# Optimization experiments

Measured on AMD Instinct MI355X. Metric: run time of the kernel, lower is better.

Reference implementation:

```python
import jax, jax.numpy as jnp
import numpy as np

MASK_GROUP = 8
RATIO = 0.125
K = max(1, min(MASK_GROUP, round(RATIO * MASK_GROUP)))  # = 1


def sparify_mask(outM):
    # top-k over the mask_group axis, scatter 1.0 at top-k positions
    _, idx = jax.lax.top_k(outM, K)              # [..., K]
    oh = jax.nn.one_hot(idx, outM.shape[-1], dtype=outM.dtype)  # [..., K, G]
    return jnp.sum(oh, axis=-2)                   # [..., G] 0/1 mask


def setup_inputs() -> dict:
    key = jax.random.key(0)
    ks = jax.random.split(key, 7)
    B, S, D, F = 4, 2048, 2048, 8192
    stdv = 1.0 / np.sqrt(F)
    u = lambda k, shape: jax.random.uniform(k, shape, jnp.float32, -stdv, stdv)
    return {
        "x": jax.random.normal(ks[0], (B, S, D), jnp.float32),
        "W1": u(ks[1], (F, D)),
        "b1": u(ks[2], (F,)),
        "Wm": u(ks[3], (MASK_GROUP, D)),
        "bm": u(ks[4], (MASK_GROUP,)),
        "W2": u(ks[5], (D, F)),
        "b2": u(ks[6], (D,)),
    }


def reference(x, W1, b1, Wm, bm, W2, b2):
    F_out = W1.shape[0]
    repeat_num = F_out // MASK_GROUP
    outL = jnp.einsum('bsd,fd->bsf', x, W1) + b1          # [B,S,F]
    outM = jax.nn.softmax(jnp.einsum('bsd,gd->bsg', x, Wm) + bm, axis=-1)  # [B,S,G]
    mask = sparify_mask(outM)                              # [B,S,G]
    gate = jnp.repeat(mask, repeat_num, axis=-1)           # [B,S,F]
    out2 = jax.nn.relu(outL * gate)
    out = jnp.einsum('bsf,df->bsd', out2, W2) + b2         # [B,S,D]
    return out
```

## Files before the change

### kernel.cpp

```cpp
#include <hip/hip_runtime.h>
#include <hip/hip_bf16.h>

#define T_TOK 8192
#define D_DIM 2048
#define F_DIM 8192
#define G_NUM 8
#define GF    1024

typedef __attribute__((ext_vector_type(8))) short bf16x8;
typedef __attribute__((ext_vector_type(4))) float f32x4;

__device__ __forceinline__ void async_load16(const void* g, void* l) {
    __builtin_amdgcn_global_load_lds(
        (const __attribute__((address_space(1))) unsigned int*)g,
        (__attribute__((address_space(3))) unsigned int*)l, 16, 0, 0);
}

__device__ __forceinline__ unsigned short f2bf(float f) {
    unsigned int u = __float_as_uint(f);
    unsigned int r = (u + 0x7fffu + ((u >> 16) & 1u)) >> 16;
    return (unsigned short)r;
}

__device__ __forceinline__ uint2 pack4(float4 v) {
    union { __hip_bfloat162 b; unsigned u; } c0, c1;
    c0.b = __float22bfloat162_rn({v.x, v.y});
    c1.b = __float22bfloat162_rn({v.z, v.w});
    uint2 r; r.x = c0.u; r.y = c1.u; return r;
}


__global__ void zero_cnt_kernel(int* __restrict__ cnt) {
    if (threadIdx.x < G_NUM) cnt[threadIdx.x] = 0;
}

__global__ __launch_bounds__(256)
void convert_kernel(const float* __restrict__ src, unsigned short* __restrict__ dst, int n) {
    int i = (blockIdx.x * 256 + threadIdx.x) * 8;
    if (i >= n) return;
    float4 a = *(const float4*)(src + i);
    float4 b = *(const float4*)(src + i + 4);
    uint2 p0 = pack4(a), p1 = pack4(b);
    uint4 o; o.x = p0.x; o.y = p0.y; o.z = p1.x; o.w = p1.y;
    *(uint4*)(dst + i) = o;
}

template <bool WRITE_XB>
__global__ __launch_bounds__(64)
void gate_partial_kernel(const float* __restrict__ x, const float* __restrict__ Wm,
                         unsigned short* __restrict__ xb, double* __restrict__ part) {
    const int q     = blockIdx.x;
    const int t     = blockIdx.y;
    const int lane  = threadIdx.x;
    const int tok0  = t * 64;
    const int kbase = q * 512;

    __shared__ float wmS[8][512];
    __shared__ float xs[64][68];

    for (int i = lane * 4; i < 8 * 512; i += 64 * 4) {
        int g = i >> 9, d = i & 511;
        *(float4*)&wmS[g][d] = *(const float4*)(Wm + (size_t)g * D_DIM + kbase + d);
    }

    double acc[8] = {0, 0, 0, 0, 0, 0, 0, 0};

    const int srow = lane >> 2;
    const int scol = (lane & 3) * 4;

    float4 v[16];
#define LOAD_CHUNK(dbase_)                                                        \
    _Pragma("unroll") for (int it = 0; it < 4; ++it)                              \
    _Pragma("unroll") for (int ci = 0; ci < 4; ++ci) {                            \
        int row = it * 16 + srow;                                                 \
        int col = ci * 16 + scol;                                                 \
        v[it * 4 + ci] = *(const float4*)(x + (size_t)(tok0 + row) * D_DIM +      \
                                          kbase + (dbase_) + col);                \
    }

    LOAD_CHUNK(0)
    __syncthreads();

    for (int s = 0; s < 8; ++s) {
        const int dbase = s * 64;
#pragma unroll
        for (int it = 0; it < 4; ++it)
#pragma unroll
            for (int ci = 0; ci < 4; ++ci) {
                int row = it * 16 + srow;
                int col = ci * 16 + scol;
                *(float4*)&xs[row][col] = v[it * 4 + ci];
                if (WRITE_XB) {
                    uint2 p = pack4(v[it * 4 + ci]);
                    *(uint2*)(xb + (size_t)(tok0 + row) * D_DIM + kbase + dbase + col) = p;
                }
            }
        __syncthreads();
        if (s < 7) { LOAD_CHUNK(dbase + 64) }
#pragma unroll
        for (int j4 = 0; j4 < 16; ++j4) {
            float4 xv = *(const float4*)&xs[lane][j4 * 4];
#pragma unroll
            for (int g = 0; g < 8; ++g) {
                float4 wv = *(const float4*)&wmS[g][dbase + j4 * 4];
                acc[g] += (double)xv.x * (double)wv.x;
                acc[g] += (double)xv.y * (double)wv.y;
                acc[g] += (double)xv.z * (double)wv.z;
                acc[g] += (double)xv.w * (double)wv.w;
            }
        }
        __syncthreads();
    }
#undef LOAD_CHUNK

    double* dst = part + (((size_t)t * 4 + q) * 64 + lane) * 8;
#pragma unroll
    for (int g = 0; g < 8; ++g) dst[g] = acc[g];
}

__global__ __launch_bounds__(256)
void gate_combine_kernel(const double* __restrict__ part, const float* __restrict__ bm,
                         int* __restrict__ cnt, int* __restrict__ bucket) {
    int tok = blockIdx.x * 256 + threadIdx.x;
    int t = tok >> 6, L = tok & 63;
    double s[8];
#pragma unroll
    for (int g = 0; g < 8; ++g) s[g] = (double)bm[g];
#pragma unroll
    for (int q = 0; q < 4; ++q) {
        const double* p = part + (((size_t)t * 4 + q) * 64 + L) * 8;
#pragma unroll
        for (int g = 0; g < 8; ++g) s[g] += p[g];
    }
    double best = s[0]; int bg = 0;
#pragma unroll
    for (int g = 1; g < 8; ++g)
        if (s[g] > best) { best = s[g]; bg = g; }
    int pos = atomicAdd(&cnt[bg], 1);
    bucket[bg * T_TOK + pos] = tok;
}

template <int KDIM, bool IS_G1, bool A_BF16, bool B_BF16>
__global__ __launch_bounds__(256)
void mfma_gemm(const void* __restrict__ Aop, const void* __restrict__ Bop,
               const float* __restrict__ bias,
               const int* __restrict__ cnt, const int* __restrict__ bucket,
               unsigned short* __restrict__ outH, float* __restrict__ outF) {
    const int g  = blockIdx.z;
    const int n  = cnt[g];
    const int t0 = blockIdx.y * 128;
    if (t0 >= n) return;
    const int nx0 = blockIdx.x * 128;
    const int tid  = threadIdx.x;
    const int lane = tid & 63;
    const int wv   = tid >> 6;

    __shared__ int toks[128];
    __shared__ __align__(16) unsigned short As[128 * 32];
    __shared__ __align__(16) unsigned short Bs[128 * 32];

    if (tid < 128) {
        int r = t0 + tid;
        if (r >= n) r = n - 1;
        toks[tid] = bucket[g * T_TOK + r];
    }
    __syncthreads();

    const size_t bstride = IS_G1 ? (size_t)KDIM : (size_t)F_DIM;
    const size_t brow0   = IS_G1 ? (size_t)(g * GF + nx0) : (size_t)nx0;
    const size_t bcol    = IS_G1 ? 0 : (size_t)(g * GF);

    const int lrow = tid >> 2;
    const int lseg = tid & 3;
    const unsigned short* aP0 = nullptr; const unsigned short* aP1 = nullptr;
    const unsigned short* bP0 = nullptr; const unsigned short* bP1 = nullptr;
    char *ldsA0 = nullptr, *ldsA1 = nullptr, *ldsB0 = nullptr, *ldsB1 = nullptr;
    if (A_BF16) {
        const unsigned short* Ab = (const unsigned short*)Aop;
        aP0 = Ab + (size_t)toks[lrow] * KDIM + lseg * 8;
        aP1 = Ab + (size_t)toks[64 + lrow] * KDIM + lseg * 8;
        ldsA0 = (char*)As + tid * 16;
        ldsA1 = (char*)As + 4096 + tid * 16;
    }
    if (B_BF16) {
        const unsigned short* Bb = (const unsigned short*)Bop;
        bP0 = Bb + (brow0 + lrow) * bstride + bcol + lseg * 8;
        bP1 = Bb + (brow0 + 64 + lrow) * bstride + bcol + lseg * 8;
        ldsB0 = (char*)Bs + tid * 16;
        ldsB1 = (char*)Bs + 4096 + tid * 16;
    }

    const int frw = tid >> 1;
    const int fsg = (tid & 1) * 16;
    const float* aF = nullptr; const float* bF = nullptr;
    char *ldsAf = nullptr, *ldsBf = nullptr;
    if (!A_BF16) {
        aF = (const float*)Aop + (size_t)toks[frw] * KDIM + fsg;
        ldsAf = (char*)As + frw * 64 + (tid & 1) * 32;
    }
    if (!B_BF16) {
        bF = (const float*)Bop + (brow0 + frw) * bstride + bcol + fsg;
        ldsBf = (char*)Bs + frw * 64 + (tid & 1) * 32;
    }

    f32x4 acc[4][4];
#pragma unroll
    for (int mi = 0; mi < 4; ++mi)
#pragma unroll
        for (int ni = 0; ni < 4; ++ni)
            acc[mi][ni] = (f32x4){0.f, 0.f, 0.f, 0.f};

    const int wr   = (wv >> 1) * 64;
    const int wc   = (wv & 1) * 64;
    const int frow = lane & 15;
    const int kh   = lane >> 4;

    for (int k0 = 0; k0 < KDIM; k0 += 32) {
        __syncthreads();
        if (A_BF16) { async_load16(aP0 + k0, ldsA0); async_load16(aP1 + k0, ldsA1); }
        if (B_BF16) { async_load16(bP0 + k0, ldsB0); async_load16(bP1 + k0, ldsB1); }
        if (!A_BF16) {
            float4 v0 = *(const float4*)(aF + k0);
            float4 v1 = *(const float4*)(aF + k0 + 4);
            float4 v2 = *(const float4*)(aF + k0 + 8);
            float4 v3 = *(const float4*)(aF + k0 + 12);
            uint2 p0 = pack4(v0), p1 = pack4(v1), p2 = pack4(v2), p3 = pack4(v3);
            uint4 w0; w0.x = p0.x; w0.y = p0.y; w0.z = p1.x; w0.w = p1.y;
            uint4 w1; w1.x = p2.x; w1.y = p2.y; w1.z = p3.x; w1.w = p3.y;
            *(uint4*)ldsAf = w0; *(uint4*)(ldsAf + 16) = w1;
        }
        if (!B_BF16) {
            float4 v0 = *(const float4*)(bF + k0);
            float4 v1 = *(const float4*)(bF + k0 + 4);
            float4 v2 = *(const float4*)(bF + k0 + 8);
            float4 v3 = *(const float4*)(bF + k0 + 12);
            uint2 p0 = pack4(v0), p1 = pack4(v1), p2 = pack4(v2), p3 = pack4(v3);
            uint4 w0; w0.x = p0.x; w0.y = p0.y; w0.z = p1.x; w0.w = p1.y;
            uint4 w1; w1.x = p2.x; w1.y = p2.y; w1.z = p3.x; w1.w = p3.y;
            *(uint4*)ldsBf = w0; *(uint4*)(ldsBf + 16) = w1;
        }
        __syncthreads();
        bf16x8 af[4], bfr[4];
#pragma unroll
        for (int mi = 0; mi < 4; ++mi)
            af[mi] = *(const bf16x8*)((const char*)As + (size_t)(wr + mi * 16 + frow) * 64 + kh * 16);
#pragma unroll
        for (int ni = 0; ni < 4; ++ni)
            bfr[ni] = *(const bf16x8*)((const char*)Bs + (size_t)(wc + ni * 16 + frow) * 64 + kh * 16);
#pragma unroll
        for (int mi = 0; mi < 4; ++mi)
#pragma unroll
            for (int ni = 0; ni < 4; ++ni)
                acc[mi][ni] = __builtin_amdgcn_mfma_f32_16x16x32_bf16(
                    af[mi], bfr[ni], acc[mi][ni], 0, 0, 0);
    }

    const float* bptr = bias + (IS_G1 ? (g * GF + nx0) : nx0);
    float bv[4];
#pragma unroll
    for (int ni = 0; ni < 4; ++ni) bv[ni] = bptr[wc + ni * 16 + frow];

#pragma unroll
    for (int mi = 0; mi < 4; ++mi) {
#pragma unroll
        for (int v = 0; v < 4; ++v) {
            int r = wr + mi * 16 + kh * 4 + v;
            if (t0 + r < n) {
                int tok = toks[r];
                if (IS_G1) {
                    unsigned short* dst = outH + (size_t)tok * GF + nx0 + wc + frow;
#pragma unroll
                    for (int ni = 0; ni < 4; ++ni) {
                        float o = fmaxf(acc[mi][ni][v] + bv[ni], 0.f);
                        dst[ni * 16] = f2bf(o);
                    }
                } else {
                    float* dst = outF + (size_t)tok * D_DIM + nx0 + wc + frow;
#pragma unroll
                    for (int ni = 0; ni < 4; ++ni)
                        dst[ni * 16] = acc[mi][ni][v] + bv[ni];
                }
            }
        }
    }
}

extern "C" void kernel_launch(void* const* d_in, const int* in_sizes, int n_in,
                              void* d_out, int out_size, void* d_ws, size_t ws_size,
                              hipStream_t stream) {
    const float* x  = (const float*)d_in[0];
    const float* W1 = (const float*)d_in[1];
    const float* b1 = (const float*)d_in[2];
    const float* Wm = (const float*)d_in[3];
    const float* bm = (const float*)d_in[4];
    const float* W2 = (const float*)d_in[5];
    const float* b2 = (const float*)d_in[6];
    float* out = (float*)d_out;

    int* cnt    = (int*)d_ws;
    int* bucket = (int*)((char*)d_ws + 1024);
    double* part = (double*)((char*)d_ws + (1 << 19));
    unsigned short* Hb  = (unsigned short*)((char*)d_ws + (1 << 19));
    unsigned short* xb  = Hb  + (size_t)T_TOK * GF;
    unsigned short* W1b = xb  + (size_t)T_TOK * D_DIM;
    unsigned short* W2b = W1b + (size_t)F_DIM * D_DIM;

    const bool fast = ws_size >= 117964800ull;
    const bool mid  = ws_size >= 50855936ull;
    const int NCVT = T_TOK * D_DIM;

    zero_cnt_kernel<<<1, 64, 0, stream>>>(cnt);
    if (fast || mid)
        gate_partial_kernel<true><<<dim3(4, 128), 64, 0, stream>>>(x, Wm, xb, part);
    else
        gate_partial_kernel<false><<<dim3(4, 128), 64, 0, stream>>>(x, Wm, nullptr, part);
    gate_combine_kernel<<<T_TOK / 256, 256, 0, stream>>>(part, bm, cnt, bucket);

    if (fast) {
        convert_kernel<<<NCVT / (256 * 8), 256, 0, stream>>>(W1, W1b, NCVT);
        convert_kernel<<<NCVT / (256 * 8), 256, 0, stream>>>(W2, W2b, NCVT);
        mfma_gemm<D_DIM, true, true, true><<<dim3(GF / 128, T_TOK / 128, G_NUM), 256, 0, stream>>>(
            xb, W1b, b1, cnt, bucket, Hb, nullptr);
        mfma_gemm<GF, false, true, true><<<dim3(D_DIM / 128, T_TOK / 128, G_NUM), 256, 0, stream>>>(
            Hb, W2b, b2, cnt, bucket, nullptr, out);
    } else if (mid) {
        mfma_gemm<D_DIM, true, true, false><<<dim3(GF / 128, T_TOK / 128, G_NUM), 256, 0, stream>>>(
            xb, W1, b1, cnt, bucket, Hb, nullptr);
        mfma_gemm<GF, false, true, false><<<dim3(D_DIM / 128, T_TOK / 128, G_NUM), 256, 0, stream>>>(
            Hb, W2, b2, cnt, bucket, nullptr, out);
    } else {
        mfma_gemm<D_DIM, true, false, false><<<dim3(GF / 128, T_TOK / 128, G_NUM), 256, 0, stream>>>(
            x, W1, b1, cnt, bucket, Hb, nullptr);
        mfma_gemm<GF, false, true, false><<<dim3(D_DIM / 128, T_TOK / 128, G_NUM), 256, 0, stream>>>(
            Hb, W2, b2, cnt, bucket, nullptr, out);
    }
}
```

Before: 405.0 us.

## Widen GEMM K-tile to 64 with XOR-swizzled LDS, remap tiles, split gate wider

The grouped MFMA GEMM now stages a 64-wide K slice per iteration, which halves the barrier count. LDS rows are XOR-swizzled to avoid bank conflicts on the fragment reads. Block indices are remapped so neighbouring blocks share token tiles for better L2 reuse. The gate partial kernel splits D into 16 chunks instead of 4 for more parallelism, and the combine kernel now sums 16 partials. In exchange, LDS use doubles per block, which may lower occupancy.

```diff
diff --git a/kernel.cpp b/kernel.cpp
--- a/kernel.cpp
+++ b/kernel.cpp
@@ -6,6 +6,8 @@
 #define F_DIM 8192
 #define G_NUM 8
 #define GF    1024
+#define GATE_Q 16
+#define GATE_D 128
 
 typedef __attribute__((ext_vector_type(8))) short bf16x8;
 typedef __attribute__((ext_vector_type(4))) float f32x4;
@@ -27,6 +29,18 @@
     c0.b = __float22bfloat162_rn({v.x, v.y});
     c1.b = __float22bfloat162_rn({v.z, v.w});
     uint2 r; r.x = c0.u; r.y = c1.u; return r;
+}
+
+__device__ __forceinline__ void stage_f32_64(const float* src, char* rowBase,
+                                             int sbase, int rmask) {
+#pragma unroll
+    for (int i = 0; i < 4; ++i) {
+        float4 v0 = *(const float4*)(src + i * 8);
+        float4 v1 = *(const float4*)(src + i * 8 + 4);
+        uint2 p0 = pack4(v0), p1 = pack4(v1);
+        uint4 w; w.x = p0.x; w.y = p0.y; w.z = p1.x; w.w = p1.y;
+        *(uint4*)(rowBase + ((sbase + i) ^ rmask) * 16) = w;
+    }
 }
 
 
@@ -53,13 +67,13 @@
     const int t     = blockIdx.y;
     const int lane  = threadIdx.x;
     const int tok0  = t * 64;
-    const int kbase = q * 512;
-
-    __shared__ float wmS[8][512];
+    const int kbase = q * GATE_D;
+
+    __shared__ float wmS[8][GATE_D];
     __shared__ float xs[64][68];
 
-    for (int i = lane * 4; i < 8 * 512; i += 64 * 4) {
-        int g = i >> 9, d = i & 511;
+    for (int i = lane * 4; i < 8 * GATE_D; i += 64 * 4) {
+        int g = i >> 7, d = i & (GATE_D - 1);
         *(float4*)&wmS[g][d] = *(const float4*)(Wm + (size_t)g * D_DIM + kbase + d);
     }
 
@@ -81,7 +95,7 @@
     LOAD_CHUNK(0)
     __syncthreads();
 
-    for (int s = 0; s < 8; ++s) {
+    for (int s = 0; s < 2; ++s) {
         const int dbase = s * 64;
 #pragma unroll
         for (int it = 0; it < 4; ++it)
@@ -96,7 +110,7 @@
                 }
             }
         __syncthreads();
-        if (s < 7) { LOAD_CHUNK(dbase + 64) }
+        if (s < 1) { LOAD_CHUNK(dbase + 64) }
 #pragma unroll
         for (int j4 = 0; j4 < 16; ++j4) {
             float4 xv = *(const float4*)&xs[lane][j4 * 4];
@@ -113,22 +127,22 @@
     }
 #undef LOAD_CHUNK
 
-    double* dst = part + (((size_t)t * 4 + q) * 64 + lane) * 8;
+    double* dst = part + (((size_t)t * GATE_Q + q) * 64 + lane) * 8;
 #pragma unroll
     for (int g = 0; g < 8; ++g) dst[g] = acc[g];
 }
 
-__global__ __launch_bounds__(256)
+__global__ __launch_bounds__(64)
 void gate_combine_kernel(const double* __restrict__ part, const float* __restrict__ bm,
                          int* __restrict__ cnt, int* __restrict__ bucket) {
-    int tok = blockIdx.x * 256 + threadIdx.x;
+    int tok = blockIdx.x * 64 + threadIdx.x;
     int t = tok >> 6, L = tok & 63;
     double s[8];
 #pragma unroll
     for (int g = 0; g < 8; ++g) s[g] = (double)bm[g];
 #pragma unroll
-    for (int q = 0; q < 4; ++q) {
-        const double* p = part + (((size_t)t * 4 + q) * 64 + L) * 8;
+    for (int q = 0; q < GATE_Q; ++q) {
+        const double* p = part + (((size_t)t * GATE_Q + q) * 64 + L) * 8;
 #pragma unroll
         for (int g = 0; g < 8; ++g) s[g] += p[g];
     }
@@ -148,16 +162,18 @@
                unsigned short* __restrict__ outH, float* __restrict__ outF) {
     const int g  = blockIdx.z;
     const int n  = cnt[g];
-    const int t0 = blockIdx.y * 128;
+    constexpr int NX = IS_G1 ? (GF / 128) : (D_DIM / 128);
+    const int l = blockIdx.y * NX + blockIdx.x;
+    const int t0  = ((l & 7) + 8 * (l / (8 * NX))) * 128;
+    const int nx0 = ((l >> 3) % NX) * 128;
     if (t0 >= n) return;
-    const int nx0 = blockIdx.x * 128;
     const int tid  = threadIdx.x;
     const int lane = tid & 63;
     const int wv   = tid >> 6;
 
     __shared__ int toks[128];
-    __shared__ __align__(16) unsigned short As[128 * 32];
-    __shared__ __align__(16) unsigned short Bs[128 * 32];
+    __shared__ __align__(16) unsigned short As[128 * 64];
+    __shared__ __align__(16) unsigned short Bs[128 * 64];
 
     if (tid < 128) {
         int r = t0 + tid;
@@ -170,38 +186,31 @@
     const size_t brow0   = IS_G1 ? (size_t)(g * GF + nx0) : (size_t)nx0;
     const size_t bcol    = IS_G1 ? 0 : (size_t)(g * GF);
 
-    const int lrow = tid >> 2;
-    const int lseg = tid & 3;
-    const unsigned short* aP0 = nullptr; const unsigned short* aP1 = nullptr;
-    const unsigned short* bP0 = nullptr; const unsigned short* bP1 = nullptr;
-    char *ldsA0 = nullptr, *ldsA1 = nullptr, *ldsB0 = nullptr, *ldsB1 = nullptr;
+    const int arow = tid >> 3;
+    const int segg = (tid & 7) ^ (arow & 7);
+    const unsigned short* aP[4]; const unsigned short* bP[4];
+    char* ldsA = (char*)As + tid * 16;
+    char* ldsB = (char*)Bs + tid * 16;
     if (A_BF16) {
         const unsigned short* Ab = (const unsigned short*)Aop;
-        aP0 = Ab + (size_t)toks[lrow] * KDIM + lseg * 8;
-        aP1 = Ab + (size_t)toks[64 + lrow] * KDIM + lseg * 8;
-        ldsA0 = (char*)As + tid * 16;
-        ldsA1 = (char*)As + 4096 + tid * 16;
+#pragma unroll
+        for (int j = 0; j < 4; ++j)
+            aP[j] = Ab + (size_t)toks[arow + 32 * j] * KDIM + segg * 8;
     }
     if (B_BF16) {
         const unsigned short* Bb = (const unsigned short*)Bop;
-        bP0 = Bb + (brow0 + lrow) * bstride + bcol + lseg * 8;
-        bP1 = Bb + (brow0 + 64 + lrow) * bstride + bcol + lseg * 8;
-        ldsB0 = (char*)Bs + tid * 16;
-        ldsB1 = (char*)Bs + 4096 + tid * 16;
+#pragma unroll
+        for (int j = 0; j < 4; ++j)
+            bP[j] = Bb + (brow0 + arow + 32 * j) * bstride + bcol + segg * 8;
     }
 
     const int frw = tid >> 1;
-    const int fsg = (tid & 1) * 16;
+    const int fs  = tid & 1;
     const float* aF = nullptr; const float* bF = nullptr;
-    char *ldsAf = nullptr, *ldsBf = nullptr;
-    if (!A_BF16) {
-        aF = (const float*)Aop + (size_t)toks[frw] * KDIM + fsg;
-        ldsAf = (char*)As + frw * 64 + (tid & 1) * 32;
-    }
-    if (!B_BF16) {
-        bF = (const float*)Bop + (brow0 + frw) * bstride + bcol + fsg;
-        ldsBf = (char*)Bs + frw * 64 + (tid & 1) * 32;
-    }
+    char* ldsAf = (char*)As + frw * 128;
+    char* ldsBf = (char*)Bs + frw * 128;
+    if (!A_BF16) aF = (const float*)Aop + (size_t)toks[frw] * KDIM + fs * 32;
+    if (!B_BF16) bF = (const float*)Bop + (brow0 + frw) * bstride + bcol + fs * 32;
 
     f32x4 acc[4][4];
 #pragma unroll
@@ -214,45 +223,40 @@
     const int wc   = (wv & 1) * 64;
     const int frow = lane & 15;
     const int kh   = lane >> 4;
-
-    for (int k0 = 0; k0 < KDIM; k0 += 32) {
+    const int xm   = frow & 7;
+    const char* aBase = (const char*)As + (size_t)(wr + frow) * 128;
+    const char* bBase = (const char*)Bs + (size_t)(wc + frow) * 128;
+
+    for (int k0 = 0; k0 < KDIM; k0 += 64) {
         __syncthreads();
-        if (A_BF16) { async_load16(aP0 + k0, ldsA0); async_load16(aP1 + k0, ldsA1); }
-        if (B_BF16) { async_load16(bP0 + k0, ldsB0); async_load16(bP1 + k0, ldsB1); }
-        if (!A_BF16) {
-            float4 v0 = *(const float4*)(aF + k0);
-            float4 v1 = *(const float4*)(aF + k0 + 4);
-            float4 v2 = *(const float4*)(aF + k0 + 8);
-            float4 v3 = *(const float4*)(aF + k0 + 12);
-            uint2 p0 = pack4(v0), p1 = pack4(v1), p2 = pack4(v2), p3 = pack4(v3);
-            uint4 w0; w0.x = p0.x; w0.y = p0.y; w0.z = p1.x; w0.w = p1.y;
-            uint4 w1; w1.x = p2.x; w1.y = p2.y; w1.z = p3.x; w1.w = p3.y;
-            *(uint4*)ldsAf = w0; *(uint4*)(ldsAf + 16) = w1;
-        }
-        if (!B_BF16) {
-            float4 v0 = *(const float4*)(bF + k0);
-            float4 v1 = *(const float4*)(bF + k0 + 4);
-            float4 v2 = *(const float4*)(bF + k0 + 8);
-            float4 v3 = *(const float4*)(bF + k0 + 12);
-            uint2 p0 = pack4(v0), p1 = pack4(v1), p2 = pack4(v2), p3 = pack4(v3);
-            uint4 w0; w0.x = p0.x; w0.y = p0.y; w0.z = p1.x; w0.w = p1.y;
-            uint4 w1; w1.x = p2.x; w1.y = p2.y; w1.z = p3.x; w1.w = p3.y;
-            *(uint4*)ldsBf = w0; *(uint4*)(ldsBf + 16) = w1;
-        }
+        if (A_BF16) {
+#pragma unroll
+            for (int j = 0; j < 4; ++j) async_load16(aP[j] + k0, ldsA + j * 4096);
+        }
+        if (B_BF16) {
+#pragma unroll
+            for (int j = 0; j < 4; ++j) async_load16(bP[j] + k0, ldsB + j * 4096);
+        }
+        if (!A_BF16) stage_f32_64(aF + k0, ldsAf, fs * 4, frw & 7);
+        if (!B_BF16) stage_f32_64(bF + k0, ldsBf, fs * 4, frw & 7);
         __syncthreads();
-        bf16x8 af[4], bfr[4];
-#pragma unroll
-        for (int mi = 0; mi < 4; ++mi)
-            af[mi] = *(const bf16x8*)((const char*)As + (size_t)(wr + mi * 16 + frow) * 64 + kh * 16);
-#pragma unroll
-        for (int ni = 0; ni < 4; ++ni)
-            bfr[ni] = *(const bf16x8*)((const char*)Bs + (size_t)(wc + ni * 16 + frow) * 64 + kh * 16);
-#pragma unroll
-        for (int mi = 0; mi < 4; ++mi)
+#pragma unroll
+        for (int kk = 0; kk < 2; ++kk) {
+            const int so = ((kk * 4 + kh) ^ xm) * 16;
+            bf16x8 af[4], bfr[4];
+#pragma unroll
+            for (int mi = 0; mi < 4; ++mi)
+                af[mi] = *(const bf16x8*)(aBase + mi * 2048 + so);
 #pragma unroll
             for (int ni = 0; ni < 4; ++ni)
-                acc[mi][ni] = __builtin_amdgcn_mfma_f32_16x16x32_bf16(
-                    af[mi], bfr[ni], acc[mi][ni], 0, 0, 0);
+                bfr[ni] = *(const bf16x8*)(bBase + ni * 2048 + so);
+#pragma unroll
+            for (int mi = 0; mi < 4; ++mi)
+#pragma unroll
+                for (int ni = 0; ni < 4; ++ni)
+                    acc[mi][ni] = __builtin_amdgcn_mfma_f32_16x16x32_bf16(
+                        af[mi], bfr[ni], acc[mi][ni], 0, 0, 0);
+        }
     }
 
     const float* bptr = bias + (IS_G1 ? (g * GF + nx0) : nx0);
@@ -311,10 +315,10 @@
 
     zero_cnt_kernel<<<1, 64, 0, stream>>>(cnt);
     if (fast || mid)
-        gate_partial_kernel<true><<<dim3(4, 128), 64, 0, stream>>>(x, Wm, xb, part);
+        gate_partial_kernel<true><<<dim3(GATE_Q, 128), 64, 0, stream>>>(x, Wm, xb, part);
     else
-        gate_partial_kernel<false><<<dim3(4, 128), 64, 0, stream>>>(x, Wm, nullptr, part);
-    gate_combine_kernel<<<T_TOK / 256, 256, 0, stream>>>(part, bm, cnt, bucket);
+        gate_partial_kernel<false><<<dim3(GATE_Q, 128), 64, 0, stream>>>(x, Wm, nullptr, part);
+    gate_combine_kernel<<<T_TOK / 64, 64, 0, stream>>>(part, bm, cnt, bucket);
 
     if (fast) {
         convert_kernel<<<NCVT / (256 * 8), 256, 0, stream>>>(W1, W1b, NCVT);
```

Result: slower. 420.1 us (+3.7%).

## Split gate reduction finer and launch grouped GEMMs from a compact tile list

Applied to the files above, without the earlier changes.

The gate partial kernel now splits the D reduction into 16 slices of 128 instead of 4 slices of 512, so it launches four times as many blocks, and the combine kernel sums the extra partials. A new single-thread kernel builds a compact list of (group, token-tile) entries from the per-group counts. Both grouped GEMMs launch only MAX_TILES rows of blocks indexed through that list, instead of a full 3D grid where most blocks exit early. The changes aim to fill the GPU during the fp64 gating pass and to cut idle block scheduling in the GEMMs. The cost is a larger partials buffer, an extra serial planning launch and more combine work.

```diff
diff --git a/kernel.cpp b/kernel.cpp
--- a/kernel.cpp
+++ b/kernel.cpp
@@ -6,6 +6,9 @@
 #define F_DIM 8192
 #define G_NUM 8
 #define GF    1024
+#define GATE_Q 16
+#define GATE_D 128
+#define MAX_TILES 72
 
 typedef __attribute__((ext_vector_type(8))) short bf16x8;
 typedef __attribute__((ext_vector_type(4))) float f32x4;
@@ -32,6 +35,17 @@
 
 __global__ void zero_cnt_kernel(int* __restrict__ cnt) {
     if (threadIdx.x < G_NUM) cnt[threadIdx.x] = 0;
+}
+
+__global__ void tile_plan_kernel(const int* __restrict__ cnt, int* __restrict__ tiles) {
+    if (threadIdx.x == 0) {
+        int k = 0;
+        for (int g = 0; g < G_NUM; ++g) {
+            int nt = (cnt[g] + 127) >> 7;
+            for (int t = 0; t < nt; ++t) tiles[k++] = (g << 16) | t;
+        }
+        for (int i = k; i < MAX_TILES; ++i) tiles[i] = -1;
+    }
 }
 
 __global__ __launch_bounds__(256)
@@ -53,13 +67,13 @@
     const int t     = blockIdx.y;
     const int lane  = threadIdx.x;
     const int tok0  = t * 64;
-    const int kbase = q * 512;
-
-    __shared__ float wmS[8][512];
+    const int kbase = q * GATE_D;
+
+    __shared__ float wmS[8][GATE_D];
     __shared__ float xs[64][68];
 
-    for (int i = lane * 4; i < 8 * 512; i += 64 * 4) {
-        int g = i >> 9, d = i & 511;
+    for (int i = lane * 4; i < 8 * GATE_D; i += 64 * 4) {
+        int g = i >> 7, d = i & (GATE_D - 1);
         *(float4*)&wmS[g][d] = *(const float4*)(Wm + (size_t)g * D_DIM + kbase + d);
     }
 
@@ -81,7 +95,7 @@
     LOAD_CHUNK(0)
     __syncthreads();
 
-    for (int s = 0; s < 8; ++s) {
+    for (int s = 0; s < 2; ++s) {
         const int dbase = s * 64;
 #pragma unroll
         for (int it = 0; it < 4; ++it)
@@ -96,7 +110,7 @@
                 }
             }
         __syncthreads();
-        if (s < 7) { LOAD_CHUNK(dbase + 64) }
+        if (s < 1) { LOAD_CHUNK(dbase + 64) }
 #pragma unroll
         for (int j4 = 0; j4 < 16; ++j4) {
             float4 xv = *(const float4*)&xs[lane][j4 * 4];
@@ -113,22 +127,22 @@
     }
 #undef LOAD_CHUNK
 
-    double* dst = part + (((size_t)t * 4 + q) * 64 + lane) * 8;
+    double* dst = part + (((size_t)t * GATE_Q + q) * 64 + lane) * 8;
 #pragma unroll
     for (int g = 0; g < 8; ++g) dst[g] = acc[g];
 }
 
-__global__ __launch_bounds__(256)
+__global__ __launch_bounds__(64)
 void gate_combine_kernel(const double* __restrict__ part, const float* __restrict__ bm,
                          int* __restrict__ cnt, int* __restrict__ bucket) {
-    int tok = blockIdx.x * 256 + threadIdx.x;
+    int tok = blockIdx.x * 64 + threadIdx.x;
     int t = tok >> 6, L = tok & 63;
     double s[8];
 #pragma unroll
     for (int g = 0; g < 8; ++g) s[g] = (double)bm[g];
 #pragma unroll
-    for (int q = 0; q < 4; ++q) {
-        const double* p = part + (((size_t)t * 4 + q) * 64 + L) * 8;
+    for (int q = 0; q < GATE_Q; ++q) {
+        const double* p = part + (((size_t)t * GATE_Q + q) * 64 + L) * 8;
 #pragma unroll
         for (int g = 0; g < 8; ++g) s[g] += p[g];
     }
@@ -145,11 +159,13 @@
 void mfma_gemm(const void* __restrict__ Aop, const void* __restrict__ Bop,
                const float* __restrict__ bias,
                const int* __restrict__ cnt, const int* __restrict__ bucket,
+               const int* __restrict__ tiles,
                unsigned short* __restrict__ outH, float* __restrict__ outF) {
-    const int g  = blockIdx.z;
+    const int e = tiles[blockIdx.y];
+    if (e < 0) return;
+    const int g  = e >> 16;
+    const int t0 = (e & 0xffff) * 128;
     const int n  = cnt[g];
-    const int t0 = blockIdx.y * 128;
-    if (t0 >= n) return;
     const int nx0 = blockIdx.x * 128;
     const int tid  = threadIdx.x;
     const int lane = tid & 63;
@@ -298,6 +314,7 @@
     float* out = (float*)d_out;
 
     int* cnt    = (int*)d_ws;
+    int* tiles  = (int*)((char*)d_ws + 64);
     int* bucket = (int*)((char*)d_ws + 1024);
     double* part = (double*)((char*)d_ws + (1 << 19));
     unsigned short* Hb  = (unsigned short*)((char*)d_ws + (1 << 19));
@@ -311,27 +328,28 @@
 
     zero_cnt_kernel<<<1, 64, 0, stream>>>(cnt);
     if (fast || mid)
-        gate_partial_kernel<true><<<dim3(4, 128), 64, 0, stream>>>(x, Wm, xb, part);
+        gate_partial_kernel<true><<<dim3(GATE_Q, 128), 64, 0, stream>>>(x, Wm, xb, part);
     else
-        gate_partial_kernel<false><<<dim3(4, 128), 64, 0, stream>>>(x, Wm, nullptr, part);
-    gate_combine_kernel<<<T_TOK / 256, 256, 0, stream>>>(part, bm, cnt, bucket);
+        gate_partial_kernel<false><<<dim3(GATE_Q, 128), 64, 0, stream>>>(x, Wm, nullptr, part);
+    gate_combine_kernel<<<T_TOK / 64, 64, 0, stream>>>(part, bm, cnt, bucket);
+    tile_plan_kernel<<<1, 64, 0, stream>>>(cnt, tiles);
 
     if (fast) {
         convert_kernel<<<NCVT / (256 * 8), 256, 0, stream>>>(W1, W1b, NCVT);
         convert_kernel<<<NCVT / (256 * 8), 256, 0, stream>>>(W2, W2b, NCVT);
-        mfma_gemm<D_DIM, true, true, true><<<dim3(GF / 128, T_TOK / 128, G_NUM), 256, 0, stream>>>(
-            xb, W1b, b1, cnt, bucket, Hb, nullptr);
-        mfma_gemm<GF, false, true, true><<<dim3(D_DIM / 128, T_TOK / 128, G_NUM), 256, 0, stream>>>(
-            Hb, W2b, b2, cnt, bucket, nullptr, out);
+        mfma_gemm<D_DIM, true, true, true><<<dim3(GF / 128, MAX_TILES), 256, 0, stream>>>(
+            xb, W1b, b1, cnt, bucket, tiles, Hb, nullptr);
+        mfma_gemm<GF, false, true, true><<<dim3(D_DIM / 128, MAX_TILES), 256, 0, stream>>>(
+            Hb, W2b, b2, cnt, bucket, tiles, nullptr, out);
     } else if (mid) {
-        mfma_gemm<D_DIM, true, true, false><<<dim3(GF / 128, T_TOK / 128, G_NUM), 256, 0, stream>>>(
-            xb, W1, b1, cnt, bucket, Hb, nullptr);
-        mfma_gemm<GF, false, true, false><<<dim3(D_DIM / 128, T_TOK / 128, G_NUM), 256, 0, stream>>>(
-            Hb, W2, b2, cnt, bucket, nullptr, out);
+        mfma_gemm<D_DIM, true, true, false><<<dim3(GF / 128, MAX_TILES), 256, 0, stream>>>(
+            xb, W1, b1, cnt, bucket, tiles, Hb, nullptr);
+        mfma_gemm<GF, false, true, false><<<dim3(D_DIM / 128, MAX_TILES), 256, 0, stream>>>(
+            Hb, W2, b2, cnt, bucket, tiles, nullptr, out);
     } else {
-        mfma_gemm<D_DIM, true, false, false><<<dim3(GF / 128, T_TOK / 128, G_NUM), 256, 0, stream>>>(
-            x, W1, b1, cnt, bucket, Hb, nullptr);
-        mfma_gemm<GF, false, true, false><<<dim3(D_DIM / 128, T_TOK / 128, G_NUM), 256, 0, stream>>>(
-            Hb, W2, b2, cnt, bucket, nullptr, out);
-    }
-}
+        mfma_gemm<D_DIM, true, false, false><<<dim3(GF / 128, MAX_TILES), 256, 0, stream>>>(
+            x, W1, b1, cnt, bucket, tiles, Hb, nullptr);
+        mfma_gemm<GF, false, true, false><<<dim3(D_DIM / 128, MAX_TILES), 256, 0, stream>>>(
+            Hb, W2, b2, cnt, bucket, tiles, nullptr, out);
+    }
+}
```

Result: no change. 402.5 us (-0.6%).
